# Optimization experiments

Hardware: AMD Instinct MI355X
Metric: run time of the kernel (lower is better)

Reference implementation:

```python
import jax, jax.numpy as jnp
import numpy as np

B, DM, NH, NL, NP = 4, 768, 12, 3, 4
HD = DM // NH
H_IMG, W_IMG = 896, 896
LEVELS = [(H_IMG // 8, W_IMG // 8), (H_IMG // 16, W_IMG // 16), (H_IMG // 32, W_IMG // 32)]
QH, QW = H_IMG // 14, W_IMG // 14
LQ = QH * QW            # 4096 query tokens (stride-14 ViT grid)
LIN = sum(h * w for h, w in LEVELS)  # 16464 multi-scale value tokens


def setup_inputs() -> dict:
    key = jax.random.key(0)
    ks = jax.random.split(key, 14)
    s = 0.02
    return {
        "query": jax.random.normal(ks[0], (B, LQ, DM), jnp.float32),
        "feat": jax.random.normal(ks[1], (B, LIN, DM), jnp.float32),
        "ln_q_g": jnp.ones((DM,), jnp.float32),
        "ln_q_b": jnp.zeros((DM,), jnp.float32),
        "ln_f_g": jnp.ones((DM,), jnp.float32),
        "ln_f_b": jnp.zeros((DM,), jnp.float32),
        "W_off": jax.random.normal(ks[2], (DM, NH * NL * NP * 2), jnp.float32) * s,
        "b_off": jax.random.normal(ks[3], (NH * NL * NP * 2,), jnp.float32) * s,
        "W_attn": jax.random.normal(ks[4], (DM, NH * NL * NP), jnp.float32) * s,
        "b_attn": jax.random.normal(ks[5], (NH * NL * NP,), jnp.float32) * s,
        "W_val": jax.random.normal(ks[6], (DM, DM), jnp.float32) * s,
        "b_val": jnp.zeros((DM,), jnp.float32),
        "W_out": jax.random.normal(ks[7], (DM, DM), jnp.float32) * s,
        "b_out": jnp.zeros((DM,), jnp.float32),
        "gamma": jax.random.normal(ks[8], (DM,), jnp.float32) * s,
    }


def _ln(x, g, b, eps=1e-6):
    m = x.mean(-1, keepdims=True)
    v = ((x - m) ** 2).mean(-1, keepdims=True)
    return (x - m) * jax.lax.rsqrt(v + eps) * g + b


def _ref_points():
    # get_reference_points for the stride-14 query grid; pixel-center coords normalized
    ry, rx = jnp.meshgrid(
        (jnp.arange(QH, dtype=jnp.float32) + 0.5) / QH,
        (jnp.arange(QW, dtype=jnp.float32) + 0.5) / QW,
        indexing="ij",
    )
    return jnp.stack([rx.reshape(-1), ry.reshape(-1)], -1)  # (LQ, 2) in (x, y)


def _sample_level(v, loc, h_, w_):
    # v: (B, h_, w_, NH, HD); loc: (B, LQ, NH, NP, 2) normalized [0,1]
    # torch grid_sample bilinear, align_corners=False, zero padding
    x = loc[..., 0] * w_ - 0.5
    y = loc[..., 1] * h_ - 0.5
    x0 = jnp.floor(x)
    y0 = jnp.floor(y)
    wx = (x - x0)[..., None]
    wy = (y - y0)[..., None]
    x0i = x0.astype(jnp.int32)
    y0i = y0.astype(jnp.int32)
    bi = jnp.arange(B)[:, None, None, None]
    hi = jnp.arange(NH)[None, None, :, None]

    def g(yi, xi):
        valid = ((xi >= 0) & (xi < w_) & (yi >= 0) & (yi < h_)).astype(v.dtype)
        got = v[bi, jnp.clip(yi, 0, h_ - 1), jnp.clip(xi, 0, w_ - 1), hi]  # (B,LQ,NH,NP,HD)
        return got * valid[..., None]

    v00 = g(y0i, x0i)
    v01 = g(y0i, x0i + 1)
    v10 = g(y0i + 1, x0i)
    v11 = g(y0i + 1, x0i + 1)
    return v00 * (1 - wx) * (1 - wy) + v01 * wx * (1 - wy) + v10 * (1 - wx) * wy + v11 * wx * wy


def _injector(query, feat, ln_q_g, ln_q_b, ln_f_g, ln_f_b, W_off, b_off, W_attn, b_attn,
              W_val, b_val, W_out, b_out, gamma):
    q = _ln(query, ln_q_g, ln_q_b)
    f = _ln(feat, ln_f_g, ln_f_b)
    value = (f @ W_val + b_val).reshape(B, LIN, NH, HD)
    off = (q @ W_off + b_off).reshape(B, LQ, NH, NL, NP, 2)
    aw = jax.nn.softmax((q @ W_attn + b_attn).reshape(B, LQ, NH, NL * NP), axis=-1)
    aw = aw.reshape(B, LQ, NH, NL, NP)
    ref = _ref_points()  # (LQ, 2)
    offset_norm = jnp.array([[w, h] for h, w in LEVELS], jnp.float32)  # (NL, 2) = (W_, H_)
    loc = ref[None, :, None, None, None, :] + off / offset_norm[None, None, None, :, None, :]
    outs = []
    start = 0
    for lvl, (h_, w_) in enumerate(LEVELS):
        v = value[:, start:start + h_ * w_].reshape(B, h_, w_, NH, HD)
        outs.append(_sample_level(v, loc[:, :, :, lvl], h_, w_))
        start += h_ * w_
    samp = jnp.stack(outs, axis=3)  # (B, LQ, NH, NL, NP, HD)
    attn_out = (samp * aw[..., None]).sum(axis=(3, 4)).reshape(B, LQ, DM)
    attn_out = attn_out @ W_out + b_out
    return query + gamma * attn_out


def reference(query, feat, ln_q_g, ln_q_b, ln_f_g, ln_f_b, W_off, b_off, W_attn, b_attn,
              W_val, b_val, W_out, b_out, gamma):
    return _injector(query, feat, ln_q_g, ln_q_b, ln_f_g, ln_f_b, W_off, b_off, W_attn,
                     b_attn, W_val, b_val, W_out, b_out, gamma)
```

## Files before the change

### kernel.cpp

```cpp
#include <hip/hip_runtime.h>
#include <hip/hip_bf16.h>

typedef __hip_bfloat16 bf16;

#define BB    4
#define LQ    4096
#define LIN   16464
#define DM    768
#define NH    12
#define HD    64
#define K_DIM 768

typedef __attribute__((ext_vector_type(8))) __bf16 bfrag;
typedef __attribute__((ext_vector_type(4))) float  ffrag;

__device__ __forceinline__ void g2l16(const void* g, void* l) {
    __builtin_amdgcn_global_load_lds(
        (const __attribute__((address_space(1))) void*)g,
        (__attribute__((address_space(3))) void*)l, 16, 0, 0);
}

__device__ __forceinline__ int xcd_swz(int orig, int nwg) {
    int xcd = orig & 7, within = orig >> 3;
    int q = nwg >> 3, r = nwg & 7;
    return (xcd < r ? xcd * (q + 1) : r * (q + 1) + (xcd - r) * q) + within;
}

__global__ __launch_bounds__(256) void ln_kernel(
    const float* __restrict__ x, const float* __restrict__ g,
    const float* __restrict__ beta, bf16* __restrict__ y)
{
    int r = blockIdx.x * 4 + (threadIdx.x >> 6);
    int lane = threadIdx.x & 63;
    const float4* xr = (const float4*)(x + (size_t)r * DM);
    float4 v[3];
    #pragma unroll
    for (int i = 0; i < 3; i++) v[i] = xr[lane + 64 * i];
    float s = 0.f, ss = 0.f;
    #pragma unroll
    for (int i = 0; i < 3; i++) {
        s  += v[i].x + v[i].y + v[i].z + v[i].w;
        ss += v[i].x * v[i].x + v[i].y * v[i].y + v[i].z * v[i].z + v[i].w * v[i].w;
    }
    #pragma unroll
    for (int m = 1; m <= 32; m <<= 1) {
        s  += __shfl_xor(s, m);
        ss += __shfl_xor(ss, m);
    }
    float mean = s * (1.f / DM);
    float inv  = rsqrtf(ss * (1.f / DM) - mean * mean + 1e-6f);
    bf16* yr = y + (size_t)r * DM;
    #pragma unroll
    for (int i = 0; i < 3; i++) {
        float4 gg = ((const float4*)g)[lane + 64 * i];
        float4 bb = ((const float4*)beta)[lane + 64 * i];
        union { bf16 h[4]; uint2 u; } p;
        p.h[0] = __float2bfloat16((v[i].x - mean) * inv * gg.x + bb.x);
        p.h[1] = __float2bfloat16((v[i].y - mean) * inv * gg.y + bb.y);
        p.h[2] = __float2bfloat16((v[i].z - mean) * inv * gg.z + bb.z);
        p.h[3] = __float2bfloat16((v[i].w - mean) * inv * gg.w + bb.w);
        *(uint2*)(yr + (lane + 64 * i) * 4) = p.u;
    }
}

__global__ __launch_bounds__(256) void cast_transpose(
    const float* __restrict__ W, bf16* __restrict__ Wt, int N)
{
    __shared__ float t[32][33];
    int n0 = blockIdx.x * 32, k0 = blockIdx.y * 32;
    int tx = threadIdx.x & 31, ty = threadIdx.x >> 5;
    #pragma unroll
    for (int i = 0; i < 4; i++) {
        int k = k0 + ty + i * 8;
        int n = n0 + tx;
        t[ty + i * 8][tx] = (n < N) ? W[(size_t)k * N + n] : 0.f;
    }
    __syncthreads();
    #pragma unroll
    for (int i = 0; i < 4; i++) {
        int n = n0 + ty + i * 8;
        Wt[(size_t)n * K_DIM + k0 + tx] = __float2bfloat16(t[tx][ty + i * 8]);
    }
}

__global__ __launch_bounds__(512) void gemm256_value(
    const bf16*  __restrict__ A,
    const bf16*  __restrict__ Bt,
    const float* __restrict__ bias,
    bf16*        __restrict__ C,
    int M, int N)
{
    __shared__ __align__(16) char lds[131072];

    int tid  = threadIdx.x;
    int lane = tid & 63;
    int wave = tid >> 6;

    int nwg  = gridDim.x * gridDim.y;
    int orig = blockIdx.y * gridDim.x + blockIdx.x;
    int wg   = xcd_swz(orig, nwg);
    int bn = (wg % gridDim.x) * 256;
    int bm = (wg / gridDim.x) * 256;

    int ahalf = wave >> 2;
    int wc    = (wave & 3) * 64;
    int bhalf = (wave & 3) >> 1;
    int bcb   = (wave & 1) * 64;

    int ln15 = lane & 15, g = lane >> 4, l7 = lane & 7;

    ffrag acc[8][4] = {};

    int r_loc = tid >> 3;
    int koff  = (((tid & 7) ^ (r_loc & 7)) * 8);

    const bf16* gA[2][2];
    const bf16* gB[2][2];
    #pragma unroll
    for (int h = 0; h < 2; h++)
        #pragma unroll
        for (int ld = 0; ld < 2; ld++) {
            int ra = min(bm + h * 128 + ld * 64 + r_loc, M - 1);
            gA[h][ld] = A  + (size_t)ra * K_DIM + koff;
            int cb = bn + h * 128 + ld * 64 + r_loc;
            gB[h][ld] = Bt + (size_t)cb * K_DIM + koff;
        }

    auto stageA = [&](char* buf, int h, int kt) {
        g2l16(gA[h][0] + kt * 64, buf + h * 16384 + tid * 16);
        g2l16(gA[h][1] + kt * 64, buf + h * 16384 + 8192 + tid * 16);
    };
    auto stageB = [&](char* buf, int h, int kt) {
        g2l16(gB[h][0] + kt * 64, buf + 32768 + h * 16384 + tid * 16);
        g2l16(gB[h][1] + kt * 64, buf + 32768 + h * 16384 + 8192 + tid * 16);
    };

    stageA(lds, 0, 0); stageA(lds, 1, 0); stageB(lds, 0, 0); stageB(lds, 1, 0);

    int sby[2];
    sby[0] = ((0 * 4 + g) ^ l7) * 16;
    sby[1] = ((1 * 4 + g) ^ l7) * 16;

    #pragma unroll
    for (int kt = 0; kt < 12; kt++) {
        char* cur = lds + (kt & 1) * 65536;
        char* nxt = lds + ((kt & 1) ^ 1) * 65536;
        const char* Ac = cur + ahalf * 16384;
        const char* Bc = cur + 32768 + bhalf * 16384;

        if (kt + 1 < 12) {
            stageA(nxt, 0, kt + 1);
            asm volatile("s_waitcnt vmcnt(2)" ::: "memory");
        } else {
            asm volatile("s_waitcnt vmcnt(0)" ::: "memory");
        }
        __builtin_amdgcn_s_barrier();

        bfrag bf[4][2];
        #pragma unroll
        for (int nc = 0; nc < 4; nc++)
            #pragma unroll
            for (int ks = 0; ks < 2; ks++)
                bf[nc][ks] = *(const bfrag*)(Bc + (bcb + nc * 16 + ln15) * 128 + sby[ks]);
        {
            bfrag af[2][2];
            #pragma unroll
            for (int m2 = 0; m2 < 2; m2++)
                #pragma unroll
                for (int ks = 0; ks < 2; ks++)
                    af[m2][ks] = *(const bfrag*)(Ac + (m2 * 16 + ln15) * 128 + sby[ks]);
            __builtin_amdgcn_s_setprio(1);
            #pragma unroll
            for (int m2 = 0; m2 < 2; m2++)
                #pragma unroll
                for (int nc = 0; nc < 4; nc++)
                    #pragma unroll
                    for (int ks = 0; ks < 2; ks++)
                        acc[m2][nc] = __builtin_amdgcn_mfma_f32_16x16x32_bf16(
                            af[m2][ks], bf[nc][ks], acc[m2][nc], 0, 0, 0);
            __builtin_amdgcn_s_setprio(0);
        }
        __builtin_amdgcn_s_barrier();

        #pragma unroll
        for (int qd = 1; qd < 4; qd++) {
            if (kt + 1 < 12) {
                if (qd == 1) stageA(nxt, 1, kt + 1);
                else if (qd == 2) stageB(nxt, 0, kt + 1);
                else stageB(nxt, 1, kt + 1);
            }
            bfrag af[2][2];
            #pragma unroll
            for (int m2 = 0; m2 < 2; m2++)
                #pragma unroll
                for (int ks = 0; ks < 2; ks++)
                    af[m2][ks] = *(const bfrag*)(Ac + ((qd * 2 + m2) * 16 + ln15) * 128 + sby[ks]);
            __builtin_amdgcn_s_setprio(1);
            #pragma unroll
            for (int m2 = 0; m2 < 2; m2++)
                #pragma unroll
                for (int nc = 0; nc < 4; nc++)
                    #pragma unroll
                    for (int ks = 0; ks < 2; ks++)
                        acc[qd * 2 + m2][nc] = __builtin_amdgcn_mfma_f32_16x16x32_bf16(
                            af[m2][ks], bf[nc][ks], acc[qd * 2 + m2][nc], 0, 0, 0);
            __builtin_amdgcn_s_setprio(0);
            __builtin_amdgcn_s_barrier();
        }
    }

    int q4 = g * 4;
    #pragma unroll
    for (int mr = 0; mr < 8; mr++) {
        #pragma unroll
        for (int rr = 0; rr < 4; rr++) {
            int rg = bm + ahalf * 128 + mr * 16 + q4 + rr;
            if (rg < M) {
                #pragma unroll
                for (int nc = 0; nc < 4; nc++) {
                    int cg = bn + wc + nc * 16 + ln15;
                    C[(size_t)rg * N + cg] =
                        __float2bfloat16(acc[mr][nc][rr] + bias[cg]);
                }
            }
        }
    }
}

__device__ __forceinline__ void gemm128_body(
    const bf16*  __restrict__ A,
    const bf16*  __restrict__ Bt,
    const float* __restrict__ bias,
    void*        __restrict__ C,
    const float* __restrict__ resid,
    const float* __restrict__ gamma,
    const float* __restrict__ bias2,
    int M, int N, int mode, int nsplit, char* lds)
{
    int tid  = threadIdx.x;
    int lane = tid & 63;

    int nwg  = gridDim.x * gridDim.y;
    int orig = blockIdx.y * gridDim.x + blockIdx.x;
    int wg = xcd_swz(orig, nwg);
    int bn = (wg % gridDim.x) * 128;
    int bm = (wg / gridDim.x) * 128;

    int wave = tid >> 6;
    int wr = (wave & 1) * 64, wc = (wave >> 1) * 64;

    ffrag acc[4][4] = {};

    int rA = tid >> 2;
    int kb = (((tid & 3) ^ ((rA >> 1) & 3)) * 8);
    int ra0 = min(bm + rA, M - 1), ra1 = min(bm + 64 + rA, M - 1);
    const bf16* gA0 = A  + (size_t)ra0 * K_DIM + kb;
    const bf16* gA1 = A  + (size_t)ra1 * K_DIM + kb;
    const bf16* gB0 = Bt + (size_t)(bn + rA) * K_DIM + kb;
    const bf16* gB1 = Bt + (size_t)(bn + 64 + rA) * K_DIM + kb;

    int mrow = lane & 15;
    int kqs  = (((lane >> 4) ^ ((mrow >> 1) & 3)) * 8);

    auto stage = [&](char* buf, int kt) {
        const int ko = kt * 32;
        g2l16(gA0 + ko, buf + tid * 16);
        g2l16(gA1 + ko, buf + tid * 16 + 4096);
        g2l16(gB0 + ko, buf + 8192 + tid * 16);
        g2l16(gB1 + ko, buf + 8192 + tid * 16 + 4096);
    };

    stage(lds, 0);
    asm volatile("s_waitcnt vmcnt(0)" ::: "memory");
    __builtin_amdgcn_s_barrier();

    #pragma unroll
    for (int kt = 0; kt < 24; kt++) {
        char* cur = lds + (kt & 1) * 16384;
        char* nxt = lds + ((kt & 1) ^ 1) * 16384;
        if (kt + 1 < 24) stage(nxt, kt + 1);

        bfrag a[4], b[4];
        #pragma unroll
        for (int t = 0; t < 4; t++) {
            a[t] = *(const bfrag*)(cur + ((wr + t * 16 + mrow) * 32 + kqs) * 2);
            b[t] = *(const bfrag*)(cur + 8192 + ((wc + t * 16 + mrow) * 32 + kqs) * 2);
        }
        __builtin_amdgcn_s_setprio(1);
        #pragma unroll
        for (int i = 0; i < 4; i++)
            #pragma unroll
            for (int j = 0; j < 4; j++)
                acc[i][j] = __builtin_amdgcn_mfma_f32_16x16x32_bf16(
                    a[i], b[j], acc[i][j], 0, 0, 0);
        __builtin_amdgcn_s_setprio(0);

        asm volatile("s_waitcnt vmcnt(0)" ::: "memory");
        __builtin_amdgcn_s_barrier();
    }

    int q4 = (lane >> 4) * 4;
    #pragma unroll
    for (int i = 0; i < 4; i++) {
        #pragma unroll
        for (int rr = 0; rr < 4; rr++) {
            int rg = bm + wr + i * 16 + q4 + rr;
            if (rg < M) {
                #pragma unroll
                for (int j = 0; j < 4; j++) {
                    int cg = bn + wc + j * 16 + mrow;
                    if (cg < N) {
                        float bv = (mode == 3 && cg >= nsplit) ? bias2[cg - nsplit]
                                                               : bias[cg];
                        float v = acc[i][j][rr] + bv;
                        size_t idx = (size_t)rg * N + cg;
                        if (mode == 2)      ((float*)C)[idx] = resid[idx] + gamma[cg] * v;
                        else                ((float*)C)[idx] = v;
                    }
                }
            }
        }
    }
}

__global__ __launch_bounds__(256) void gemm128_comb(
    const bf16* __restrict__ A, const bf16* __restrict__ Bt,
    const float* __restrict__ bias, void* __restrict__ C,
    const float* __restrict__ bias2, int M, int N, int nsplit)
{
    __shared__ __align__(16) char lds[32768];
    gemm128_body(A, Bt, bias, C, nullptr, nullptr, bias2, M, N, 3, nsplit, lds);
}

__global__ __launch_bounds__(256) void gemm128_out(
    const bf16* __restrict__ A, const bf16* __restrict__ Bt,
    const float* __restrict__ bias, void* __restrict__ C,
    const float* __restrict__ resid, const float* __restrict__ gamma,
    int M, int N)
{
    __shared__ __align__(16) char lds[32768];
    gemm128_body(A, Bt, bias, C, resid, gamma, nullptr, M, N, 2, 0, lds);
}

__global__ __launch_bounds__(256) void sample_kernel(
    const bf16*  __restrict__ value,
    const float* __restrict__ comb,
    bf16*        __restrict__ attn)
{
    int wg = xcd_swz(blockIdx.x, gridDim.x);
    int unit = __builtin_amdgcn_readfirstlane((wg << 2) + (threadIdx.x >> 6));
    int lane = threadIdx.x & 63;
    int o   = lane & 7;
    int c8  = lane >> 3;
    int k   = c8 & 3;
    int dx  = k & 1, dy = k >> 1;
    int h  = unit % NH;
    int bq = unit / NH;
    int q  = bq & (LQ - 1);
    int b  = bq >> 12;

    const float* rowp = comb + (size_t)bq * 432;
    const float* ob = rowp + h * 24;
    const float* lg = rowp + 288 + h * 12;

    float l[12];
    float mx = -1e30f;
    #pragma unroll
    for (int i = 0; i < 12; i++) { l[i] = lg[i]; mx = fmaxf(mx, l[i]); }
    float den = 0.f;
    #pragma unroll
    for (int i = 0; i < 12; i++) { l[i] = __expf(l[i] - mx); den += l[i]; }
    float rden = 1.f / den;
    #pragma unroll
    for (int i = 0; i < 12; i++) l[i] *= rden;

    float rx = ((q & 63) + 0.5f) * (1.f / 64.f);
    float ry = ((q >> 6) + 0.5f) * (1.f / 64.f);

    float acc[8] = {0.f};

    #pragma unroll
    for (int it = 0; it < 6; it++) {
        const int wl = (it < 2) ? 112 : (it < 4 ? 56 : 28);
        const int sl = (it < 2) ? 0   : (it < 4 ? 12544 : 15680);
        int s = it * 2 + ((lane >> 5) & 1);
        float ox = ob[s * 2 + 0];
        float oy = ob[s * 2 + 1];
        float x = rx * wl + ox - 0.5f;
        float y = ry * wl + oy - 0.5f;
        float xf = floorf(x), yf = floorf(y);
        float wx = x - xf,  wy = y - yf;
        int xi = (int)xf + dx;
        int yi = (int)yf + dy;
        bool valid = ((unsigned)xi < (unsigned)wl) & ((unsigned)yi < (unsigned)wl);
        int xc = min(max(xi, 0), wl - 1);
        int yc = min(max(yi, 0), wl - 1);
        int cell = b * LIN + sl + yc * wl + xc;
        const uint4* vp = (const uint4*)(value + ((size_t)cell * NH + h) * HD + o * 8);
        uint4 v = *vp;
        float aw = (lane & 32) ? l[it * 2 + 1] : l[it * 2];
        float bw = (dx ? wx : 1.f - wx) * (dy ? wy : 1.f - wy);
        float w = valid ? aw * bw : 0.f;
        const unsigned* u = (const unsigned*)&v;
        #pragma unroll
        for (int j = 0; j < 4; j++) {
            float f0 = __uint_as_float(u[j] << 16);
            float f1 = __uint_as_float(u[j] & 0xFFFF0000u);
            acc[j * 2 + 0] = fmaf(w, f0, acc[j * 2 + 0]);
            acc[j * 2 + 1] = fmaf(w, f1, acc[j * 2 + 1]);
        }
    }

    #pragma unroll
    for (int m = 8; m <= 32; m <<= 1) {
        #pragma unroll
        for (int j = 0; j < 8; j++)
            acc[j] += __shfl_xor(acc[j], m);
    }

    if (c8 == 0) {
        union { bf16 h8[8]; uint4 u4; } r;
        #pragma unroll
        for (int j = 0; j < 8; j++) r.h8[j] = __float2bfloat16(acc[j]);
        *(uint4*)(attn + (size_t)bq * DM + h * HD + o * 8) = r.u4;
    }
}

extern "C" void kernel_launch(void* const* d_in, const int* in_sizes, int n_in,
                              void* d_out, int out_size, void* d_ws, size_t ws_size,
                              hipStream_t stream)
{
    const float* query  = (const float*)d_in[0];
    const float* feat   = (const float*)d_in[1];
    const float* ln_q_g = (const float*)d_in[2];
    const float* ln_q_b = (const float*)d_in[3];
    const float* ln_f_g = (const float*)d_in[4];
    const float* ln_f_b = (const float*)d_in[5];
    const float* W_off  = (const float*)d_in[6];
    const float* b_off  = (const float*)d_in[7];
    const float* W_attn = (const float*)d_in[8];
    const float* b_attn = (const float*)d_in[9];
    const float* W_val  = (const float*)d_in[10];
    const float* b_val  = (const float*)d_in[11];
    const float* W_out  = (const float*)d_in[12];
    const float* b_out  = (const float*)d_in[13];
    const float* gamma  = (const float*)d_in[14];
    float* out = (float*)d_out;

    char* ws = (char*)d_ws;
    char* od = (char*)d_out;
    const int M_F = BB * LIN;
    const int M_Q = BB * LQ;

    bf16*  value  = (bf16*)(ws);
    bf16*  f_ln   = (bf16*)(ws + 101154816);
    bf16*  Wt_out = (bf16*)(ws + 101154816);
    bf16*  q_ln   = (bf16*)(ws + 202309632);
    bf16*  attn   = (bf16*)(ws + 202309632);

    bf16*  Wt_val  = (bf16*)(od);
    bf16*  Wt_comb = (bf16*)(od + 1179648);
    float* comb    = (float*)(od + 2162688);

    cast_transpose<<<dim3(24, 24), 256, 0, stream>>>(W_val, Wt_val, 768);
    cast_transpose<<<dim3(9, 24), 256, 0, stream>>>(W_off, Wt_comb, 288);
    cast_transpose<<<dim3(7, 24), 256, 0, stream>>>(
        W_attn, Wt_comb + (size_t)288 * K_DIM, 144);

    ln_kernel<<<M_F / 4, 256, 0, stream>>>(feat, ln_f_g, ln_f_b, f_ln);
    ln_kernel<<<M_Q / 4, 256, 0, stream>>>(query, ln_q_g, ln_q_b, q_ln);

    gemm256_value<<<dim3(3, (M_F + 255) / 256), 512, 0, stream>>>(
        f_ln, Wt_val, b_val, value, M_F, DM);

    cast_transpose<<<dim3(24, 24), 256, 0, stream>>>(W_out, Wt_out, 768);

    gemm128_comb<<<dim3(4, M_Q / 128), 256, 0, stream>>>(
        q_ln, Wt_comb, b_off, comb, b_attn, M_Q, 432, 288);

    sample_kernel<<<(M_Q * NH) / 4, 256, 0, stream>>>(value, comb, attn);

    gemm128_out<<<dim3(6, M_Q / 128), 256, 0, stream>>>(
        attn, Wt_out, b_out, out, query, gamma, M_Q, DM);
}
```

Baseline: 702.6 us.

## Remap sampling lanes to 16 corners×points and reduce via LDS instead of shuffles

Reassigns lanes in the deformable sampling kernel so that each lane handles one (point, corner) pair per level. Each lane now loads 32 bytes of the head vector, and the loop runs 3 iterations instead of 6. The cross-lane shuffle reduction is replaced by a swizzled per-wave LDS transpose-and-sum that writes one bf16 per lane. Softmax normalisation is folded into the bilinear weight, and the XCD block swizzle is dropped. The LDS path relies only on an lgkmcnt wait inside the wave, with no barrier, which is valid because each wave reduces only its own slice.

```diff
diff --git a/kernel.cpp b/kernel.cpp
--- a/kernel.cpp
+++ b/kernel.cpp
@@ -347,13 +347,15 @@
     const float* __restrict__ comb,
     bf16*        __restrict__ attn)
 {
-    int wg = xcd_swz(blockIdx.x, gridDim.x);
-    int unit = __builtin_amdgcn_readfirstlane((wg << 2) + (threadIdx.x >> 6));
+    __shared__ float red[4][16][64];
+
+    int wv   = threadIdx.x >> 6;
+    int unit = __builtin_amdgcn_readfirstlane((blockIdx.x << 2) + wv);
     int lane = threadIdx.x & 63;
-    int o   = lane & 7;
-    int c8  = lane >> 3;
-    int k   = c8 & 3;
-    int dx  = k & 1, dy = k >> 1;
+    int c16  = lane >> 2;
+    int o4   = lane & 3;
+    int pt2  = c16 >> 2;
+    int dx   = c16 & 1, dy = (c16 >> 1) & 1;
     int h  = unit % NH;
     int bq = unit / NH;
     int q  = bq & (LQ - 1);
@@ -363,67 +365,77 @@
     const float* ob = rowp + h * 24;
     const float* lg = rowp + 288 + h * 12;
 
-    float l[12];
-    float mx = -1e30f;
-    #pragma unroll
-    for (int i = 0; i < 12; i++) { l[i] = lg[i]; mx = fmaxf(mx, l[i]); }
+    float4 lv0 = ((const float4*)lg)[0];
+    float4 lv1 = ((const float4*)lg)[1];
+    float4 lv2 = ((const float4*)lg)[2];
+    float l[12] = {lv0.x, lv0.y, lv0.z, lv0.w,
+                   lv1.x, lv1.y, lv1.z, lv1.w,
+                   lv2.x, lv2.y, lv2.z, lv2.w};
+    float mx = fmaxf(fmaxf(fmaxf(fmaxf(l[0], l[1]), fmaxf(l[2], l[3])),
+                           fmaxf(fmaxf(l[4], l[5]), fmaxf(l[6], l[7]))),
+                     fmaxf(fmaxf(l[8], l[9]), fmaxf(l[10], l[11])));
     float den = 0.f;
     #pragma unroll
     for (int i = 0; i < 12; i++) { l[i] = __expf(l[i] - mx); den += l[i]; }
     float rden = 1.f / den;
-    #pragma unroll
-    for (int i = 0; i < 12; i++) l[i] *= rden;
 
     float rx = ((q & 63) + 0.5f) * (1.f / 64.f);
     float ry = ((q >> 6) + 0.5f) * (1.f / 64.f);
 
-    float acc[8] = {0.f};
-
-    #pragma unroll
-    for (int it = 0; it < 6; it++) {
-        const int wl = (it < 2) ? 112 : (it < 4 ? 56 : 28);
-        const int sl = (it < 2) ? 0   : (it < 4 ? 12544 : 15680);
-        int s = it * 2 + ((lane >> 5) & 1);
-        float ox = ob[s * 2 + 0];
-        float oy = ob[s * 2 + 1];
+    float acc[16] = {0.f};
+
+    #pragma unroll
+    for (int g = 0; g < 3; g++) {
+        const int wl = (g == 0) ? 112 : (g == 1 ? 56 : 28);
+        const int sl = (g == 0) ? 0   : (g == 1 ? 12544 : 15680);
+        int s2 = (g * 4 + pt2) * 2;
+        float ox = ob[s2], oy = ob[s2 + 1];
+        float awA = (pt2 & 1) ? l[g * 4 + 1] : l[g * 4 + 0];
+        float awB = (pt2 & 1) ? l[g * 4 + 3] : l[g * 4 + 2];
+        float aw  = (pt2 & 2) ? awB : awA;
+
         float x = rx * wl + ox - 0.5f;
         float y = ry * wl + oy - 0.5f;
         float xf = floorf(x), yf = floorf(y);
-        float wx = x - xf,  wy = y - yf;
+        float wxf = x - xf, wyf = y - yf;
         int xi = (int)xf + dx;
         int yi = (int)yf + dy;
         bool valid = ((unsigned)xi < (unsigned)wl) & ((unsigned)yi < (unsigned)wl);
         int xc = min(max(xi, 0), wl - 1);
         int yc = min(max(yi, 0), wl - 1);
         int cell = b * LIN + sl + yc * wl + xc;
-        const uint4* vp = (const uint4*)(value + ((size_t)cell * NH + h) * HD + o * 8);
-        uint4 v = *vp;
-        float aw = (lane & 32) ? l[it * 2 + 1] : l[it * 2];
-        float bw = (dx ? wx : 1.f - wx) * (dy ? wy : 1.f - wy);
-        float w = valid ? aw * bw : 0.f;
-        const unsigned* u = (const unsigned*)&v;
+        const uint4* vp = (const uint4*)(value
+            + (unsigned)(cell * NH + h) * HD + o4 * 16);
+        uint4 v0 = vp[0];
+        uint4 v1 = vp[1];
+        float bw = (dx ? wxf : 1.f - wxf) * (dy ? wyf : 1.f - wyf);
+        float w  = valid ? aw * (bw * rden) : 0.f;
+        const unsigned* u0 = (const unsigned*)&v0;
+        const unsigned* u1 = (const unsigned*)&v1;
         #pragma unroll
         for (int j = 0; j < 4; j++) {
-            float f0 = __uint_as_float(u[j] << 16);
-            float f1 = __uint_as_float(u[j] & 0xFFFF0000u);
-            acc[j * 2 + 0] = fmaf(w, f0, acc[j * 2 + 0]);
-            acc[j * 2 + 1] = fmaf(w, f1, acc[j * 2 + 1]);
-        }
-    }
-
-    #pragma unroll
-    for (int m = 8; m <= 32; m <<= 1) {
-        #pragma unroll
-        for (int j = 0; j < 8; j++)
-            acc[j] += __shfl_xor(acc[j], m);
-    }
-
-    if (c8 == 0) {
-        union { bf16 h8[8]; uint4 u4; } r;
-        #pragma unroll
-        for (int j = 0; j < 8; j++) r.h8[j] = __float2bfloat16(acc[j]);
-        *(uint4*)(attn + (size_t)bq * DM + h * HD + o * 8) = r.u4;
-    }
+            acc[j * 2 + 0] = fmaf(w, __uint_as_float(u0[j] << 16),        acc[j * 2 + 0]);
+            acc[j * 2 + 1] = fmaf(w, __uint_as_float(u0[j] & 0xFFFF0000u), acc[j * 2 + 1]);
+            acc[8 + j * 2 + 0] = fmaf(w, __uint_as_float(u1[j] << 16),        acc[8 + j * 2 + 0]);
+            acc[8 + j * 2 + 1] = fmaf(w, __uint_as_float(u1[j] & 0xFFFF0000u), acc[8 + j * 2 + 1]);
+        }
+    }
+
+    float* rw = &red[wv][c16][0];
+    #pragma unroll
+    for (int bi = 0; bi < 4; bi++) {
+        int col = (o4 * 16 + bi * 4 + c16 * 4) & 63;
+        *(float4*)&rw[col] = float4{acc[bi * 4 + 0], acc[bi * 4 + 1],
+                                    acc[bi * 4 + 2], acc[bi * 4 + 3]};
+    }
+    asm volatile("s_waitcnt lgkmcnt(0)" ::: "memory");
+    __builtin_amdgcn_sched_barrier(0);
+    float sum = 0.f;
+    #pragma unroll
+    for (int s = 0; s < 16; s++)
+        sum += red[wv][s][(lane + s * 4) & 63];
+
+    attn[(size_t)bq * DM + h * HD + lane] = __float2bfloat16(sum);
 }
 
 extern "C" void kernel_launch(void* const* d_in, const int* in_sizes, int n_in,
```

Result: slower. 752.5 us (+7.1%).
